# Kernel optimization log

Measured on AMD Instinct MI355X. Metric: run time of the kernel, lower is better.

Reference implementation:

```python
import jax, jax.numpy as jnp
import numpy as np

N = 100000      # num_nodes
E = 1600000     # num_edges
F_IN = 5        # in_features
H = 64          # hidden_channels
HC = H // 2     # classifier hidden
L = 3           # num GCN layers
EPS = 1e-5      # BatchNorm eps


def setup_inputs() -> dict:
    key = jax.random.key(0)
    ks = jax.random.split(key, 12)
    s = 0.1
    return {
        "x": jax.random.normal(ks[0], (N, F_IN), dtype=jnp.float32),
        "edge_index": jax.random.randint(ks[1], (2, E), 0, N, dtype=jnp.int32),
        "W_in": jax.random.normal(ks[2], (F_IN, H), dtype=jnp.float32) * s,
        "b_in": jax.random.normal(ks[3], (H,), dtype=jnp.float32) * s,
        "conv_W": jax.random.normal(ks[4], (L, H, H), dtype=jnp.float32) * s,
        "conv_b": jax.random.normal(ks[5], (L, H), dtype=jnp.float32) * s,
        "bn_gamma": jnp.ones((L, H), dtype=jnp.float32),
        "bn_beta": jnp.zeros((L, H), dtype=jnp.float32),
        "W1": jax.random.normal(ks[6], (H, HC), dtype=jnp.float32) * s,
        "b1": jax.random.normal(ks[7], (HC,), dtype=jnp.float32) * s,
        "W2": jax.random.normal(ks[8], (HC, 1), dtype=jnp.float32) * s,
        "b2": jax.random.normal(ks[9], (1,), dtype=jnp.float32) * s,
    }


def reference(x, edge_index, W_in, b_in, conv_W, conv_b, bn_gamma, bn_beta, W1, b1, W2, b2):
    src, dst = edge_index[0], edge_index[1]

    # input projection + ReLU
    h = jax.nn.relu(x @ W_in + b_in)  # (N, H)

    # GCN symmetric normalization with self-loops (PyG GCNConv default):
    # deg includes the self-loop weight of 1.
    deg = jax.ops.segment_sum(jnp.ones((E,), dtype=h.dtype), dst, num_segments=N) + 1.0
    dinv = jax.lax.rsqrt(deg)                       # deg^{-1/2}, (N,)
    edge_coef = dinv[src] * dinv[dst]               # (E,)
    self_coef = dinv * dinv                         # (N,)

    for i in range(L):
        hw = h @ conv_W[i]                          # linear (no bias yet), (N, H)
        # gather -> scale -> scatter-add aggregation, plus self-loop term
        agg = jax.ops.segment_sum(hw[src] * edge_coef[:, None], dst, num_segments=N)
        agg = agg + hw * self_coef[:, None] + conv_b[i]
        # BatchNorm1d over nodes (batch statistics; eval dropout = identity)
        mean = jnp.mean(agg, axis=0)
        var = jnp.var(agg, axis=0)
        h = bn_gamma[i] * (agg - mean) * jax.lax.rsqrt(var + EPS) + bn_beta[i]
        h = jax.nn.relu(h)

    # classifier MLP: H -> H//2 -> 1, squeeze to (N,)
    logits = (jax.nn.relu(h @ W1 + b1) @ W2 + b2).squeeze(-1)
    return logits
```

## Files before the change

### kernel.cpp

```cpp
#include <hip/hip_runtime.h>

#define NN 100000
#define EE 1600000
#define EPSV 1e-5f

__device__ __forceinline__ unsigned short f2bf(float f) {
    union { float f; unsigned int u; } cv;
    cv.f = f;
    unsigned int u = cv.u;
    u += 0x7FFFu + ((u >> 16) & 1u);
    return (unsigned short)(u >> 16);
}

__device__ __forceinline__ float bf2f(unsigned short u) {
    union { unsigned int i; float f; } cv;
    cv.i = ((unsigned int)u) << 16;
    return cv.f;
}

__global__ void deg_kernel(const int* __restrict__ dst, int* __restrict__ degi) {
    int e = blockIdx.x * 256 + threadIdx.x;
    if (e < EE) atomicAdd(&degi[dst[e]], 1);
}

__global__ void dinv_kernel(const int* __restrict__ degi, float* __restrict__ dinv) {
    int n = blockIdx.x * 256 + threadIdx.x;
    if (n < NN) dinv[n] = rsqrtf((float)degi[n] + 1.0f);
}

__global__ void scan1(const int* __restrict__ degi, int* __restrict__ offsets,
                      int* __restrict__ partial) {
    __shared__ int sdata[256];
    int t = threadIdx.x;
    int n = blockIdx.x * 256 + t;
    int v = (n < NN) ? degi[n] : 0;
    sdata[t] = v;
    __syncthreads();
    for (int off = 1; off < 256; off <<= 1) {
        int x = (t >= off) ? sdata[t - off] : 0;
        __syncthreads();
        sdata[t] += x;
        __syncthreads();
    }
    if (n < NN) offsets[n] = sdata[t] - v;
    if (t == 255) partial[blockIdx.x] = sdata[255];
}

__global__ void scan2(int* __restrict__ partial, int* __restrict__ partial_pref, int nparts) {
    __shared__ int sdata[512];
    int t = threadIdx.x;
    int v = (t < nparts) ? partial[t] : 0;
    sdata[t] = v;
    __syncthreads();
    for (int off = 1; off < 512; off <<= 1) {
        int x = (t >= off) ? sdata[t - off] : 0;
        __syncthreads();
        sdata[t] += x;
        __syncthreads();
    }
    if (t < nparts) partial_pref[t] = sdata[t] - v;
}

__global__ void scan3(int* __restrict__ offsets, const int* __restrict__ partial_pref) {
    int n = blockIdx.x * 256 + threadIdx.x;
    if (n < NN) offsets[n] += partial_pref[n >> 8];
}

__global__ void fill_kernel(const int* __restrict__ src, const int* __restrict__ dst,
                            int* __restrict__ offsets, const float* __restrict__ dinv,
                            int2* __restrict__ sorted) {
    int e = blockIdx.x * 256 + threadIdx.x;
    if (e >= EE) return;
    int s = src[e], d = dst[e];
    int idx = atomicAdd(&offsets[d], 1);
    int2 rec;
    rec.x = s;
    rec.y = __float_as_int(dinv[s] * dinv[d]);
    sorted[idx] = rec;
}

__global__ __launch_bounds__(256) void gemm64_bn(const float* __restrict__ in,
                                                 const float* __restrict__ x,
                                                 const float* __restrict__ Win,
                                                 const float* __restrict__ bin,
                                                 const float* __restrict__ stats,
                                                 const float* __restrict__ gamma,
                                                 const float* __restrict__ beta,
                                                 const float* __restrict__ W,
                                                 unsigned short* __restrict__ out,
                                                 int mode) {
    __shared__ __align__(16) float Ws[4096];
    __shared__ float Hs[64 * 65];
    __shared__ float scale[64], shift[64];
    __shared__ float Wins[320];
    __shared__ float bins[64];
    int t = threadIdx.x;
    if (mode == 1) {
        if (t < 64) {
            const float invN = 1.0f / (float)NN;
            float mean = stats[t] * invN;
            float var = stats[64 + t] * invN - mean * mean;
            float rstd = rsqrtf(var + EPSV);
            float sc = gamma[t] * rstd;
            scale[t] = sc;
            shift[t] = beta[t] - mean * sc;
        }
    } else {
        for (int i = t; i < 320; i += 256) Wins[i] = Win[i];
        if (t < 64) bins[t] = bin[t];
    }
    for (int i = t; i < 4096; i += 256) Ws[i] = W[i];
    __syncthreads();
    int base = blockIdx.x * 64;
    if (mode == 1) {
        for (int i = t; i < 4096; i += 256) {
            int r = i >> 6, c = i & 63;
            float v = 0.f;
            if (base + r < NN) {
                v = in[(base + r) * 64 + c];
                v = fmaxf(v * scale[c] + shift[c], 0.f);
            }
            Hs[r * 65 + c] = v;
        }
    } else {
        for (int i = t; i < 4096; i += 256) {
            int r = i >> 6, c = i & 63;
            int n = base + r;
            float v = 0.f;
            if (n < NN) {
                float acc = bins[c];
#pragma unroll
                for (int k = 0; k < 5; ++k) acc += x[n * 5 + k] * Wins[k * 64 + c];
                v = fmaxf(acc, 0.f);
            }
            Hs[r * 65 + c] = v;
        }
    }
    __syncthreads();
    int c0 = (t & 15) * 4;
    int r0 = (t >> 4) * 4;
    float acc[4][4] = {};
    for (int k = 0; k < 64; ++k) {
        float4 w = *(const float4*)&Ws[k * 64 + c0];
        float hv[4];
#pragma unroll
        for (int j = 0; j < 4; ++j) hv[j] = Hs[(r0 + j) * 65 + k];
#pragma unroll
        for (int j = 0; j < 4; ++j) {
            acc[j][0] += hv[j] * w.x;
            acc[j][1] += hv[j] * w.y;
            acc[j][2] += hv[j] * w.z;
            acc[j][3] += hv[j] * w.w;
        }
    }
#pragma unroll
    for (int j = 0; j < 4; ++j) {
        int n = base + r0 + j;
        if (n < NN) {
            ushort4 pk;
            pk.x = f2bf(acc[j][0]);
            pk.y = f2bf(acc[j][1]);
            pk.z = f2bf(acc[j][2]);
            pk.w = f2bf(acc[j][3]);
            *(ushort4*)&out[n * 64 + c0] = pk;
        }
    }
}

__global__ __launch_bounds__(256) void agg_kernel(const unsigned short* __restrict__ hw,
                                                  const int2* __restrict__ sorted,
                                                  const int* __restrict__ offsets,
                                                  const int* __restrict__ degi,
                                                  const float* __restrict__ dinv,
                                                  const float* __restrict__ b,
                                                  float* __restrict__ agg,
                                                  float* __restrict__ stats) {
    int t = threadIdx.x;
    int c = t & 63;
    int w = t >> 6;
    float bc = b[c];
    float bsum = 0.f, bss = 0.f;
    for (int n = blockIdx.x * 4 + w; n < NN; n += gridDim.x * 4) {
        int cnt = degi[n];
        int start = offsets[n] - cnt;
        float di = dinv[n];
        float acc = bf2f(hw[n * 64 + c]) * (di * di) + bc;
        for (int base = 0; base < cnt; base += 64) {
            int m = min(64, cnt - base);
            int2 rec = make_int2(0, 0);
            if (c < m) rec = sorted[start + base + c];
            int k = 0;
            for (; k + 8 <= m; k += 8) {
                int s0 = __shfl(rec.x, k);
                int s1 = __shfl(rec.x, k + 1);
                int s2 = __shfl(rec.x, k + 2);
                int s3 = __shfl(rec.x, k + 3);
                int s4 = __shfl(rec.x, k + 4);
                int s5 = __shfl(rec.x, k + 5);
                int s6 = __shfl(rec.x, k + 6);
                int s7 = __shfl(rec.x, k + 7);
                float v0 = bf2f(hw[s0 * 64 + c]);
                float v1 = bf2f(hw[s1 * 64 + c]);
                float v2 = bf2f(hw[s2 * 64 + c]);
                float v3 = bf2f(hw[s3 * 64 + c]);
                float v4 = bf2f(hw[s4 * 64 + c]);
                float v5 = bf2f(hw[s5 * 64 + c]);
                float v6 = bf2f(hw[s6 * 64 + c]);
                float v7 = bf2f(hw[s7 * 64 + c]);
                float c0 = __int_as_float(__shfl(rec.y, k));
                float c1 = __int_as_float(__shfl(rec.y, k + 1));
                float c2 = __int_as_float(__shfl(rec.y, k + 2));
                float c3 = __int_as_float(__shfl(rec.y, k + 3));
                float c4 = __int_as_float(__shfl(rec.y, k + 4));
                float c5 = __int_as_float(__shfl(rec.y, k + 5));
                float c6 = __int_as_float(__shfl(rec.y, k + 6));
                float c7 = __int_as_float(__shfl(rec.y, k + 7));
                acc += v0 * c0;
                acc += v1 * c1;
                acc += v2 * c2;
                acc += v3 * c3;
                acc += v4 * c4;
                acc += v5 * c5;
                acc += v6 * c6;
                acc += v7 * c7;
            }
            for (; k < m; ++k) {
                int s = __shfl(rec.x, k);
                float cf = __int_as_float(__shfl(rec.y, k));
                acc += bf2f(hw[s * 64 + c]) * cf;
            }
        }
        agg[n * 64 + c] = acc;
        bsum += acc;
        bss += acc * acc;
    }
    __shared__ float red[2][4][64];
    red[0][w][c] = bsum;
    red[1][w][c] = bss;
    __syncthreads();
    if (w == 0) {
        float s = red[0][0][c] + red[0][1][c] + red[0][2][c] + red[0][3][c];
        float ss = red[1][0][c] + red[1][1][c] + red[1][2][c] + red[1][3][c];
        atomicAdd(&stats[c], s);
        atomicAdd(&stats[64 + c], ss);
    }
}

__global__ __launch_bounds__(256) void classifier(const float* __restrict__ agg,
                                                  const float* __restrict__ stats,
                                                  const float* __restrict__ gamma,
                                                  const float* __restrict__ beta,
                                                  const float* __restrict__ W1,
                                                  const float* __restrict__ b1,
                                                  const float* __restrict__ W2,
                                                  const float* __restrict__ b2,
                                                  float* __restrict__ out) {
    __shared__ float W1s[2048];
    __shared__ float b1s[32];
    __shared__ float W2s[32];
    __shared__ float scale[64], shift[64];
    int t = threadIdx.x;
    for (int i = t; i < 2048; i += 256) W1s[i] = W1[i];
    if (t < 32) {
        b1s[t] = b1[t];
        W2s[t] = W2[t];
    }
    if (t < 64) {
        const float invN = 1.0f / (float)NN;
        float mean = stats[t] * invN;
        float var = stats[64 + t] * invN - mean * mean;
        float rstd = rsqrtf(var + EPSV);
        float sc = gamma[t] * rstd;
        scale[t] = sc;
        shift[t] = beta[t] - mean * sc;
    }
    __syncthreads();
    int n = blockIdx.x * 256 + t;
    if (n >= NN) return;
    float4 h4[16];
    const float4* hp = (const float4*)(agg + n * 64);
#pragma unroll
    for (int i = 0; i < 16; ++i) h4[i] = hp[i];
    float* hr = (float*)h4;
#pragma unroll
    for (int k = 0; k < 64; ++k) hr[k] = fmaxf(hr[k] * scale[k] + shift[k], 0.f);
    float o = b2[0];
    for (int c = 0; c < 32; ++c) {
        float z = b1s[c];
#pragma unroll
        for (int k = 0; k < 64; ++k) z += hr[k] * W1s[k * 32 + c];
        o += fmaxf(z, 0.f) * W2s[c];
    }
    out[n] = o;
}

extern "C" void kernel_launch(void* const* d_in, const int* in_sizes, int n_in,
                              void* d_out, int out_size, void* d_ws, size_t ws_size,
                              hipStream_t stream) {
    const float* x    = (const float*)d_in[0];
    const int*   ei   = (const int*)d_in[1];
    const float* Win  = (const float*)d_in[2];
    const float* bin  = (const float*)d_in[3];
    const float* cW   = (const float*)d_in[4];
    const float* cb   = (const float*)d_in[5];
    const float* gam  = (const float*)d_in[6];
    const float* bet  = (const float*)d_in[7];
    const float* W1   = (const float*)d_in[8];
    const float* b1   = (const float*)d_in[9];
    const float* W2   = (const float*)d_in[10];
    const float* b2   = (const float*)d_in[11];
    float* out = (float*)d_out;

    unsigned short* hw = (unsigned short*)d_ws;
    float* agg   = (float*)d_ws + NN * 32;
    float* dinv  = agg + NN * 64;
    float* stats = dinv + NN;
    int*  degi        = (int*)(stats + 3 * 128);
    int*  offsets     = degi + NN;
    int2* sorted      = (int2*)(offsets + NN);

    int* partial      = (int*)agg;
    int* partial_pref = (int*)agg + 512;

    const int* src = ei;
    const int* dst = ei + EE;

    const int NB = (NN + 255) / 256;

    (void)hipMemsetAsync(degi, 0, NN * sizeof(int), stream);
    (void)hipMemsetAsync(stats, 0, 3 * 128 * sizeof(float), stream);

    deg_kernel<<<(EE + 255) / 256, 256, 0, stream>>>(dst, degi);
    dinv_kernel<<<NB, 256, 0, stream>>>(degi, dinv);
    scan1<<<NB, 256, 0, stream>>>(degi, offsets, partial);
    scan2<<<1, 512, 0, stream>>>(partial, partial_pref, NB);
    scan3<<<NB, 256, 0, stream>>>(offsets, partial_pref);
    fill_kernel<<<(EE + 255) / 256, 256, 0, stream>>>(src, dst, offsets, dinv, sorted);

    for (int i = 0; i < 3; ++i) {
        gemm64_bn<<<(NN + 63) / 64, 256, 0, stream>>>(
            agg, x, Win, bin, stats + (i - 1) * 128, gam + (i - 1) * 64,
            bet + (i - 1) * 64, cW + i * 4096, hw, i > 0 ? 1 : 0);
        agg_kernel<<<2048, 256, 0, stream>>>(hw, sorted, offsets, degi, dinv,
                                             cb + i * 64, agg, stats + i * 128);
    }

    classifier<<<(NN + 255) / 256, 256, 0, stream>>>(agg, stats + 2 * 128, gam + 2 * 64,
                                                     bet + 2 * 64, W1, b1, W2, b2, out);
}
```

Before: 604.6 us.

## Split hw into four 16-channel planes and aggregate one plane per block

The GEMM now writes hw as four separate 16-channel bf16 planes, each packed as 8 uint32 per node. The aggregation kernel assigns a quarter of the channels to each block. Every wave handles 8 neighbors at a time, each 8-lane group loading one 32-byte row slice, and the partial sums are reduced with xor shuffles. The goal is to shrink the gather footprint each block touches (one 3.2MB plane instead of 12.8MB) for better cache locality, and to use wider per-lane loads. The cost is extra shuffle reductions, a grid that depends on a hardcoded stride of 2048, and lane underuse on the final write.

```diff
diff --git a/kernel.cpp b/kernel.cpp
--- a/kernel.cpp
+++ b/kernel.cpp
@@ -87,7 +87,7 @@
                                                  const float* __restrict__ gamma,
                                                  const float* __restrict__ beta,
                                                  const float* __restrict__ W,
-                                                 unsigned short* __restrict__ out,
+                                                 unsigned int* __restrict__ out32,
                                                  int mode) {
     __shared__ __align__(16) float Ws[4096];
     __shared__ float Hs[64 * 65];
@@ -153,21 +153,22 @@
             acc[j][3] += hv[j] * w.w;
         }
     }
+    int q = c0 >> 4;
+    int u0 = (c0 & 15) >> 1;
+    unsigned int* dstq = out32 + (size_t)q * NN * 8;
 #pragma unroll
     for (int j = 0; j < 4; ++j) {
         int n = base + r0 + j;
         if (n < NN) {
-            ushort4 pk;
-            pk.x = f2bf(acc[j][0]);
-            pk.y = f2bf(acc[j][1]);
-            pk.z = f2bf(acc[j][2]);
-            pk.w = f2bf(acc[j][3]);
-            *(ushort4*)&out[n * 64 + c0] = pk;
-        }
-    }
-}
-
-__global__ __launch_bounds__(256) void agg_kernel(const unsigned short* __restrict__ hw,
+            uint2 pk;
+            pk.x = (unsigned int)f2bf(acc[j][0]) | ((unsigned int)f2bf(acc[j][1]) << 16);
+            pk.y = (unsigned int)f2bf(acc[j][2]) | ((unsigned int)f2bf(acc[j][3]) << 16);
+            *(uint2*)&dstq[n * 8 + u0] = pk;
+        }
+    }
+}
+
+__global__ __launch_bounds__(256) void agg_kernel(const unsigned int* __restrict__ hw32,
                                                   const int2* __restrict__ sorted,
                                                   const int* __restrict__ offsets,
                                                   const int* __restrict__ degi,
@@ -176,73 +177,66 @@
                                                   float* __restrict__ agg,
                                                   float* __restrict__ stats) {
     int t = threadIdx.x;
-    int c = t & 63;
+    int lane = t & 63;
     int w = t >> 6;
-    float bc = b[c];
-    float bsum = 0.f, bss = 0.f;
-    for (int n = blockIdx.x * 4 + w; n < NN; n += gridDim.x * 4) {
+    int g = lane >> 3;
+    int u = lane & 7;
+    int q = blockIdx.x & 3;
+    const unsigned int* hq = hw32 + (size_t)q * NN * 8;
+    int cq0 = q * 16;
+    float b0 = b[cq0 + 2 * u], b1v = b[cq0 + 2 * u + 1];
+    float bsx = 0.f, bsy = 0.f, bqx = 0.f, bqy = 0.f;
+    for (int n = (blockIdx.x >> 2) * 4 + w; n < NN; n += 2048) {
         int cnt = degi[n];
         int start = offsets[n] - cnt;
         float di = dinv[n];
-        float acc = bf2f(hw[n * 64 + c]) * (di * di) + bc;
+        float ax = 0.f, ay = 0.f;
         for (int base = 0; base < cnt; base += 64) {
             int m = min(64, cnt - base);
             int2 rec = make_int2(0, 0);
-            if (c < m) rec = sorted[start + base + c];
-            int k = 0;
-            for (; k + 8 <= m; k += 8) {
-                int s0 = __shfl(rec.x, k);
-                int s1 = __shfl(rec.x, k + 1);
-                int s2 = __shfl(rec.x, k + 2);
-                int s3 = __shfl(rec.x, k + 3);
-                int s4 = __shfl(rec.x, k + 4);
-                int s5 = __shfl(rec.x, k + 5);
-                int s6 = __shfl(rec.x, k + 6);
-                int s7 = __shfl(rec.x, k + 7);
-                float v0 = bf2f(hw[s0 * 64 + c]);
-                float v1 = bf2f(hw[s1 * 64 + c]);
-                float v2 = bf2f(hw[s2 * 64 + c]);
-                float v3 = bf2f(hw[s3 * 64 + c]);
-                float v4 = bf2f(hw[s4 * 64 + c]);
-                float v5 = bf2f(hw[s5 * 64 + c]);
-                float v6 = bf2f(hw[s6 * 64 + c]);
-                float v7 = bf2f(hw[s7 * 64 + c]);
-                float c0 = __int_as_float(__shfl(rec.y, k));
-                float c1 = __int_as_float(__shfl(rec.y, k + 1));
-                float c2 = __int_as_float(__shfl(rec.y, k + 2));
-                float c3 = __int_as_float(__shfl(rec.y, k + 3));
-                float c4 = __int_as_float(__shfl(rec.y, k + 4));
-                float c5 = __int_as_float(__shfl(rec.y, k + 5));
-                float c6 = __int_as_float(__shfl(rec.y, k + 6));
-                float c7 = __int_as_float(__shfl(rec.y, k + 7));
-                acc += v0 * c0;
-                acc += v1 * c1;
-                acc += v2 * c2;
-                acc += v3 * c3;
-                acc += v4 * c4;
-                acc += v5 * c5;
-                acc += v6 * c6;
-                acc += v7 * c7;
+            if (lane < m) rec = sorted[start + base + lane];
+            int nGrp = (m + 7) >> 3;
+#pragma unroll 2
+            for (int grp = 0; grp < nGrp; ++grp) {
+                int idx = grp * 8 + g;
+                int s = __shfl(rec.x, idx);
+                float cf = __int_as_float(__shfl(rec.y, idx));
+                unsigned int uv = hq[s * 8 + u];
+                ax += bf2f((unsigned short)(uv & 0xffffu)) * cf;
+                ay += bf2f((unsigned short)(uv >> 16)) * cf;
             }
-            for (; k < m; ++k) {
-                int s = __shfl(rec.x, k);
-                float cf = __int_as_float(__shfl(rec.y, k));
-                acc += bf2f(hw[s * 64 + c]) * cf;
-            }
-        }
-        agg[n * 64 + c] = acc;
-        bsum += acc;
-        bss += acc * acc;
-    }
-    __shared__ float red[2][4][64];
-    red[0][w][c] = bsum;
-    red[1][w][c] = bss;
-    __syncthreads();
-    if (w == 0) {
-        float s = red[0][0][c] + red[0][1][c] + red[0][2][c] + red[0][3][c];
-        float ss = red[1][0][c] + red[1][1][c] + red[1][2][c] + red[1][3][c];
-        atomicAdd(&stats[c], s);
-        atomicAdd(&stats[64 + c], ss);
+        }
+        ax += __shfl_xor(ax, 8);
+        ay += __shfl_xor(ay, 8);
+        ax += __shfl_xor(ax, 16);
+        ay += __shfl_xor(ay, 16);
+        ax += __shfl_xor(ax, 32);
+        ay += __shfl_xor(ay, 32);
+        if (lane < 8) {
+            unsigned int us = hq[n * 8 + u];
+            float sc = di * di;
+            float vx = ax + bf2f((unsigned short)(us & 0xffffu)) * sc + b0;
+            float vy = ay + bf2f((unsigned short)(us >> 16)) * sc + b1v;
+            *(float2*)&agg[n * 64 + cq0 + 2 * u] = make_float2(vx, vy);
+            bsx += vx;
+            bsy += vy;
+            bqx += vx * vx;
+            bqy += vy * vy;
+        }
+    }
+    __shared__ float red[2][4][16];
+    if (lane < 8) {
+        red[0][w][2 * u] = bsx;
+        red[0][w][2 * u + 1] = bsy;
+        red[1][w][2 * u] = bqx;
+        red[1][w][2 * u + 1] = bqy;
+    }
+    __syncthreads();
+    if (w == 0 && t < 16) {
+        float s = red[0][0][t] + red[0][1][t] + red[0][2][t] + red[0][3][t];
+        float ss = red[1][0][t] + red[1][1][t] + red[1][2][t] + red[1][3][t];
+        atomicAdd(&stats[cq0 + t], s);
+        atomicAdd(&stats[64 + cq0 + t], ss);
     }
 }
 
@@ -311,7 +305,7 @@
     const float* b2   = (const float*)d_in[11];
     float* out = (float*)d_out;
 
-    unsigned short* hw = (unsigned short*)d_ws;
+    unsigned int* hw = (unsigned int*)d_ws;
     float* agg   = (float*)d_ws + NN * 32;
     float* dinv  = agg + NN * 64;
     float* stats = dinv + NN;
```

New measurement: 697.7 us. 15.4% more time.
